# Performance work log

Hardware: AMD Instinct MI355X
Metric: run time of the kernel (lower is better)

## Reference

```python
import jax, jax.numpy as jnp
import numpy as np

SOFTCAP = 30.0

def setup_inputs() -> dict:
    key = jax.random.key(0)
    ks = jax.random.split(key, 5)
    T, D, F, E = 8192, 2048, 4096, 8
    s_in = 1.0 / np.sqrt(D)
    s_mid = 1.0 / np.sqrt(F)
    return {
        "hidden_states": jax.random.normal(ks[0], (T, D), jnp.float32),
        "gate_w": jax.random.normal(ks[1], (D, E), jnp.float32) * s_in,
        "w_gate": jax.random.normal(ks[2], (E, D, F), jnp.float32) * s_in,
        "w_up": jax.random.normal(ks[3], (E, D, F), jnp.float32) * s_in,
        "w_down": jax.random.normal(ks[4], (E, F, D), jnp.float32) * s_mid,
        "top_k": 2,
    }

def reference(hidden_states, gate_w, w_gate, w_up, w_down, top_k):
    x = hidden_states
    T = x.shape[0]
    # --- router: fp32 gate, tanh softcap, softmax ---
    logits = x.astype(jnp.float32) @ gate_w                      # [T, E]
    logits = jnp.tanh(logits / SOFTCAP) * SOFTCAP
    probs = jax.nn.softmax(logits, axis=-1)                      # [T, E]
    # --- top-k selection (weights are the softmax probs, no renorm) ---
    weights, idx = jax.lax.top_k(probs, top_k)                   # [T, k]
    combine = jnp.zeros_like(probs).at[jnp.arange(T)[:, None], idx].set(
        weights.astype(probs.dtype))                              # [T, E]
    combine = combine.astype(x.dtype)
    # --- expert MLPs: gelu(x@w_gate) * (x@w_up) @ w_down, scan over E ---
    def step(acc, ewts):
        wg, wu, wd, c = ewts                                     # [D,F],[D,F],[F,D],[T]
        h = jax.nn.gelu(x @ wg) * (x @ wu)                       # [T, F]
        return acc + c[:, None] * (h @ wd), None
    out, _ = jax.lax.scan(step, jnp.zeros_like(x),
                          (w_gate, w_up, w_down, combine.T))
    return out
```

## Files before the change

kernel.cpp:

```cpp
#include <hip/hip_runtime.h>
#include <hip/hip_bf16.h>
#include <cstdint>
#include <cstddef>

#define TNUM 8192
#define DDIM 2048
#define FDIM 4096
#define NEXP 8

typedef __attribute__((ext_vector_type(4))) float f32x4;
typedef __attribute__((ext_vector_type(4))) unsigned u32x4;
typedef __attribute__((ext_vector_type(8))) short s16x8;
typedef __attribute__((ext_vector_type(8))) __bf16 bf16x8v;

__device__ inline f32x4 mfma16(s16x8 a, s16x8 b, f32x4 c) {
  return __builtin_amdgcn_mfma_f32_16x16x32_bf16(
      __builtin_bit_cast(bf16x8v, a), __builtin_bit_cast(bf16x8v, b), c, 0, 0, 0);
}

__device__ inline unsigned short bf16r(float f) {
  union { float f; unsigned u; } x; x.f = f;
  unsigned r = x.u + 0x7fffu + ((x.u >> 16) & 1u);
  return (unsigned short)(r >> 16);
}

__device__ inline unsigned pk2(float a, float b) {
  __hip_bfloat162 h = __float22bfloat162_rn(make_float2(a, b));
  unsigned r;
  __builtin_memcpy(&r, &h, 4);
  return r;
}

__device__ inline int swz16(int row, int b) {
  return (row << 7) + (b ^ ((row & 7) << 4));
}

typedef const __attribute__((address_space(1))) void* gp_t;
typedef __attribute__((address_space(3))) void* lp_t;
__device__ inline void gl16(const void* g, void* l) {
  __builtin_amdgcn_global_load_lds((gp_t)g, (lp_t)l, 16, 0, 0);
}

#define FENCE asm volatile("" ::: "memory")

__global__ __launch_bounds__(256) void k_router(
    const float* __restrict__ x, const float* __restrict__ gw,
    int* __restrict__ top_idx, float* __restrict__ top_w, int* __restrict__ counts) {
  __shared__ float gwT[NEXP][DDIM];
  const int tid = threadIdx.x;
  for (int i = tid; i < NEXP * DDIM; i += 256) {
    int d = i >> 3, e = i & 7;
    gwT[e][d] = gw[i];
  }
  __syncthreads();
  const int lane = tid & 63;
  const int t = blockIdx.x * 4 + (tid >> 6);
  const float4* xr = (const float4*)(x + (size_t)t * DDIM);
  double acc[NEXP];
#pragma unroll
  for (int e = 0; e < NEXP; e++) acc[e] = 0.0;
  for (int d4 = lane; d4 < DDIM / 4; d4 += 64) {
    float4 xv = xr[d4];
#pragma unroll
    for (int e = 0; e < NEXP; e++) {
      float4 gv = *(const float4*)&gwT[e][d4 * 4];
      acc[e] += (double)xv.x * gv.x + (double)xv.y * gv.y +
                (double)xv.z * gv.z + (double)xv.w * gv.w;
    }
  }
#pragma unroll
  for (int e = 0; e < NEXP; e++) {
    double v = acc[e];
#pragma unroll
    for (int s = 32; s > 0; s >>= 1) v += __shfl_xor(v, s);
    acc[e] = v;
  }
  if (lane == 0) {
    int i0 = 0; double b0 = acc[0];
#pragma unroll
    for (int e = 1; e < NEXP; e++) if (acc[e] > b0) { b0 = acc[e]; i0 = e; }
    int i1 = (i0 == 0) ? 1 : 0; double b1 = acc[i1];
#pragma unroll
    for (int e = 0; e < NEXP; e++) {
      if (e == i0 || e == i1) continue;
      if (acc[e] > b1) { b1 = acc[e]; i1 = e; }
    }
    float lc[NEXP]; float mx = -1e30f;
#pragma unroll
    for (int e = 0; e < NEXP; e++) {
      lc[e] = tanhf((float)(acc[e] * (1.0 / 30.0))) * 30.0f;
      mx = lc[e] > mx ? lc[e] : mx;
    }
    float s = 0.0f;
#pragma unroll
    for (int e = 0; e < NEXP; e++) { lc[e] = expf(lc[e] - mx); s += lc[e]; }
    float inv = 1.0f / s;
    top_idx[t * 2] = i0; top_idx[t * 2 + 1] = i1;
    top_w[t * 2] = lc[i0] * inv; top_w[t * 2 + 1] = lc[i1] * inv;
    atomicAdd(&counts[i0], 1);
    atomicAdd(&counts[i1], 1);
  }
}

__global__ void k_scan(const int* __restrict__ counts, int* __restrict__ offs,
                       int* __restrict__ cursor) {
  if (threadIdx.x == 0) {
    int s = 0;
    for (int e = 0; e < NEXP; e++) { offs[e] = s; cursor[e] = s; s += counts[e]; }
    offs[NEXP] = s;
  }
}

__global__ void k_scatter(const int* __restrict__ top_idx, const float* __restrict__ top_w,
                          int* __restrict__ cursor, int* __restrict__ perm_tok,
                          float* __restrict__ perm_w) {
  int t = blockIdx.x * 256 + threadIdx.x;
#pragma unroll
  for (int k = 0; k < 2; k++) {
    int e = top_idx[t * 2 + k];
    int pos = atomicAdd(&cursor[e], 1);
    perm_tok[pos] = t;
    perm_w[pos] = top_w[t * 2 + k];
  }
}

__global__ void k_cast(const float* __restrict__ x, unsigned short* __restrict__ xb) {
  size_t i = ((size_t)blockIdx.x * 256 + threadIdx.x) * 8;
  f32x4 a = *(const f32x4*)(x + i);
  f32x4 b = *(const f32x4*)(x + i + 4);
  u32x4 v;
  v[0] = pk2(a[0], a[1]); v[1] = pk2(a[2], a[3]);
  v[2] = pk2(b[0], b[1]); v[3] = pk2(b[2], b[3]);
  *(u32x4*)(xb + i) = v;
}

__global__ __launch_bounds__(256) void k_convT(
    const float* __restrict__ src, unsigned short* __restrict__ dst,
    int K, int N, int cmap) {
  __shared__ char ct[8192];
  const int e = blockIdx.z;
  const float* src_e = src + (size_t)e * K * N;
  const int nout = cmap ? 2 * N : N;
  unsigned short* dst_e = dst + (size_t)e * nout * K;
  const int k0 = blockIdx.y * 64, n0 = blockIdx.x * 64;
  const int tid = threadIdx.x;
#pragma unroll
  for (int i = 0; i < 4; i++) {
    int idx = tid + i * 256;
    int kr = idx >> 4, f4 = idx & 15;
    f32x4 v = *(const f32x4*)(src_e + (size_t)(k0 + kr) * N + n0 + f4 * 4);
#pragma unroll
    for (int j = 0; j < 4; j++) {
      int n = f4 * 4 + j;
      *(unsigned short*)(ct + n * 128 + ((kr * 2) ^ ((n & 7) << 4))) = bf16r(v[j]);
    }
  }
  __syncthreads();
#pragma unroll
  for (int i = 0; i < 2; i++) {
    int s = tid + i * 256;
    int n = s >> 3, ks = s & 7;
    int gn = n0 + n;
    int cd = cmap ? (((gn >> 4) << 5) + (gn & 15) + (cmap == 2 ? 16 : 0)) : gn;
    s16x8 val = *(const s16x8*)(ct + n * 128 + ((ks * 16) ^ ((n & 7) << 4)));
    *(s16x8*)(dst_e + (size_t)cd * K + k0 + ks * 8) = val;
  }
}

__global__ __launch_bounds__(512, 2) void k_mlp1(
    const unsigned short* __restrict__ xb, const unsigned short* __restrict__ wguT,
    const int* __restrict__ perm_tok, const int* __restrict__ offs,
    unsigned short* __restrict__ H) {
  extern __shared__ char lds[];
  const int e = blockIdx.z;
  const int off = offs[e], cnt = offs[e + 1] - off;
  const int nb = blockIdx.x * 256;
  const unsigned short* wgu_e = wguT + (size_t)e * 2 * DDIM * FDIM;
  const int tid = threadIdx.x;
  const int lane = tid & 63;
  const int wid = tid >> 6;
  const int wr = wid >> 2, wc = wid & 3;
  const int l15 = lane & 15, lk = lane >> 4;
  const int wbase = wid * 1024;

#pragma unroll 1
  for (int mt = blockIdx.y; mt * 256 < cnt; mt += 8) {
    const unsigned short* asrc[4];
    const unsigned short* bsrc[4];
#pragma unroll
    for (int i = 0; i < 4; i++) {
      int seg = tid + i * 512;
      int m = seg >> 3, kp = (seg & 7) ^ (m & 7);
      int gm = mt * 256 + m;
      if (gm >= cnt) gm = cnt - 1;
      asrc[i] = xb + (size_t)perm_tok[off + gm] * DDIM + kp * 8;
      bsrc[i] = wgu_e + (size_t)(nb + m) * DDIM + kp * 8;
    }
    f32x4 acc[8][4];
#pragma unroll
    for (int mi = 0; mi < 8; mi++)
#pragma unroll
      for (int ni = 0; ni < 4; ni++) acc[mi][ni] = f32x4{0.f, 0.f, 0.f, 0.f};

#define STAGE1(buf, koff)                                        \
    {                                                            \
      char* As_ = lds + (buf) * 65536;                           \
      char* Bs_ = As_ + 32768;                                   \
      _Pragma("unroll") for (int i = 0; i < 4; i++) {            \
        gl16(asrc[i] + (koff), As_ + i * 8192 + wbase);          \
        gl16(bsrc[i] + (koff), Bs_ + i * 8192 + wbase);          \
      }                                                          \
    }

    STAGE1(0, 0);
    int cur = 0;
#pragma unroll 1
    for (int t = 0; t < DDIM / 64; t++) {
      if (t + 1 < DDIM / 64) {
        STAGE1(cur ^ 1, (t + 1) * 64);
        asm volatile("s_waitcnt vmcnt(8)" ::: "memory");
      } else {
        asm volatile("s_waitcnt vmcnt(0)" ::: "memory");
      }
      FENCE;
      __builtin_amdgcn_s_barrier();
      FENCE;
      {
        char* As_ = lds + cur * 65536;
        char* Bs_ = As_ + 32768;
        __builtin_amdgcn_s_setprio(1);
#pragma unroll
        for (int ks = 0; ks < 2; ks++) {
          s16x8 b[4];
#pragma unroll
          for (int ni = 0; ni < 4; ni++)
            b[ni] = *(const s16x8*)(Bs_ + swz16(wc * 64 + ni * 16 + l15, ks * 64 + lk * 16));
#pragma unroll
          for (int mih = 0; mih < 2; mih++) {
            s16x8 a[4];
#pragma unroll
            for (int mi = 0; mi < 4; mi++)
              a[mi] = *(const s16x8*)(As_ + swz16(wr * 128 + mih * 64 + mi * 16 + l15,
                                                 ks * 64 + lk * 16));
#pragma unroll
            for (int ni = 0; ni < 4; ni++)
#pragma unroll
              for (int mi = 0; mi < 4; mi++)
                acc[mih * 4 + mi][ni] = mfma16(a[mi], b[ni], acc[mih * 4 + mi][ni]);
          }
        }
        __builtin_amdgcn_s_setprio(0);
      }
      FENCE;
      __builtin_amdgcn_s_barrier();
      FENCE;
      cur ^= 1;
    }
#undef STAGE1

#pragma unroll
    for (int am = 0; am < 8; am++) {
      int rb = wr * 128 + am * 16 + lk * 4;
#pragma unroll
      for (int j = 0; j < 4; j++) {
        int gm = mt * 256 + rb + j;
        if (gm < cnt) {
          unsigned short* hrow = H + (size_t)(off + gm) * FDIM;
#pragma unroll
          for (int ni = 0; ni < 4; ni += 2) {
            int jj = (nb >> 4) + wc * 4 + ni;
            int hc = ((jj >> 1) << 4) + l15;
            float g = acc[am][ni][j];
            float u = acc[am][ni + 1][j];
            float x3 = g * g * g;
            float gl = 0.5f * g * (1.0f + tanhf(0.7978845608f * (g + 0.044715f * x3)));
            hrow[hc] = bf16r(gl * u);
          }
        }
      }
    }
  }
}

__global__ __launch_bounds__(512, 2) void k_mlp2(
    const unsigned short* __restrict__ H, const unsigned short* __restrict__ wdT,
    const int* __restrict__ perm_tok, const float* __restrict__ perm_w,
    const int* __restrict__ offs, float* __restrict__ out) {
  extern __shared__ char lds[];
  const int e = blockIdx.z;
  const int off = offs[e], cnt = offs[e + 1] - off;
  const int nb = blockIdx.x * 256;
  const unsigned short* wd_e = wdT + (size_t)e * FDIM * DDIM;
  const int tid = threadIdx.x;
  const int lane = tid & 63;
  const int wid = tid >> 6;
  const int wr = wid >> 2, wc = wid & 3;
  const int l15 = lane & 15, lk = lane >> 4;
  const int wbase = wid * 1024;

#pragma unroll 1
  for (int mt = blockIdx.y; mt * 256 < cnt; mt += 8) {
    const unsigned short* asrc[4];
    const unsigned short* bsrc[4];
#pragma unroll
    for (int i = 0; i < 4; i++) {
      int seg = tid + i * 512;
      int m = seg >> 3, kp = (seg & 7) ^ (m & 7);
      int gm = mt * 256 + m;
      if (gm >= cnt) gm = cnt - 1;
      asrc[i] = H + (size_t)(off + gm) * FDIM + kp * 8;
      bsrc[i] = wd_e + (size_t)(nb + m) * FDIM + kp * 8;
    }
    f32x4 acc[8][4];
#pragma unroll
    for (int mi = 0; mi < 8; mi++)
#pragma unroll
      for (int ni = 0; ni < 4; ni++) acc[mi][ni] = f32x4{0.f, 0.f, 0.f, 0.f};

#define STAGE2(buf, koff)                                        \
    {                                                            \
      char* As_ = lds + (buf) * 65536;                           \
      char* Bs_ = As_ + 32768;                                   \
      _Pragma("unroll") for (int i = 0; i < 4; i++) {            \
        gl16(asrc[i] + (koff), As_ + i * 8192 + wbase);          \
        gl16(bsrc[i] + (koff), Bs_ + i * 8192 + wbase);          \
      }                                                          \
    }

    STAGE2(0, 0);
    int cur = 0;
#pragma unroll 1
    for (int t = 0; t < FDIM / 64; t++) {
      if (t + 1 < FDIM / 64) {
        STAGE2(cur ^ 1, (t + 1) * 64);
        asm volatile("s_waitcnt vmcnt(8)" ::: "memory");
      } else {
        asm volatile("s_waitcnt vmcnt(0)" ::: "memory");
      }
      FENCE;
      __builtin_amdgcn_s_barrier();
      FENCE;
      {
        char* As_ = lds + cur * 65536;
        char* Bs_ = As_ + 32768;
        __builtin_amdgcn_s_setprio(1);
#pragma unroll
        for (int ks = 0; ks < 2; ks++) {
          s16x8 b[4];
#pragma unroll
          for (int ni = 0; ni < 4; ni++)
            b[ni] = *(const s16x8*)(Bs_ + swz16(wc * 64 + ni * 16 + l15, ks * 64 + lk * 16));
#pragma unroll
          for (int mih = 0; mih < 2; mih++) {
            s16x8 a[4];
#pragma unroll
            for (int mi = 0; mi < 4; mi++)
              a[mi] = *(const s16x8*)(As_ + swz16(wr * 128 + mih * 64 + mi * 16 + l15,
                                                 ks * 64 + lk * 16));
#pragma unroll
            for (int ni = 0; ni < 4; ni++)
#pragma unroll
              for (int mi = 0; mi < 4; mi++)
                acc[mih * 4 + mi][ni] = mfma16(a[mi], b[ni], acc[mih * 4 + mi][ni]);
          }
        }
        __builtin_amdgcn_s_setprio(0);
      }
      FENCE;
      __builtin_amdgcn_s_barrier();
      FENCE;
      cur ^= 1;
    }
#undef STAGE2

#pragma unroll
    for (int am = 0; am < 8; am++) {
      int rb = wr * 128 + am * 16 + lk * 4;
#pragma unroll
      for (int j = 0; j < 4; j++) {
        int gm = mt * 256 + rb + j;
        if (gm < cnt) {
          int tok = perm_tok[off + gm];
          float w = perm_w[off + gm];
          float* orow = out + (size_t)tok * DDIM + nb + wc * 64 + l15;
#pragma unroll
          for (int ni = 0; ni < 4; ni++) atomicAdd(&orow[ni * 16], w * acc[am][ni][j]);
        }
      }
    }
  }
}

extern "C" void kernel_launch(void* const* d_in, const int* in_sizes, int n_in,
                              void* d_out, int out_size, void* d_ws, size_t ws_size,
                              hipStream_t stream) {
  const float* x = (const float*)d_in[0];
  const float* gw = (const float*)d_in[1];
  const float* wgate = (const float*)d_in[2];
  const float* wup = (const float*)d_in[3];
  const float* wdown = (const float*)d_in[4];
  float* out = (float*)d_out;

  const size_t XB_B = 33554432;
  const size_t H_B = 134217728;
  const size_t WGU_B = 268435456;
  const size_t WD_B = 134217728;

  char* ws = (char*)d_ws;
  unsigned short* xb = (unsigned short*)ws;
  unsigned short* H = (unsigned short*)(ws + XB_B);
  unsigned short* wguT = (unsigned short*)(ws + XB_B + H_B);
  unsigned short* wdT = (unsigned short*)(ws + XB_B + H_B + WGU_B);
  char* meta = ws + XB_B + H_B + WGU_B + WD_B;
  int* counts = (int*)(meta);
  int* offs = (int*)(meta + 64);
  int* cursor = (int*)(meta + 128);
  int* top_idx = (int*)(meta + 256);
  float* top_w = (float*)(meta + 256 + 65536);
  int* perm_tok = (int*)(meta + 256 + 131072);
  float* perm_w = (float*)(meta + 256 + 196608);

  (void)hipFuncSetAttribute((const void*)k_mlp1,
                            hipFuncAttributeMaxDynamicSharedMemorySize, 131072);
  (void)hipFuncSetAttribute((const void*)k_mlp2,
                            hipFuncAttributeMaxDynamicSharedMemorySize, 131072);

  (void)hipMemsetAsync(counts, 0, 64, stream);
  (void)hipMemsetAsync(d_out, 0, (size_t)TNUM * DDIM * 4, stream);
  k_router<<<TNUM / 4, 256, 0, stream>>>(x, gw, top_idx, top_w, counts);
  k_scan<<<1, 64, 0, stream>>>(counts, offs, cursor);
  k_scatter<<<TNUM / 256, 256, 0, stream>>>(top_idx, top_w, cursor, perm_tok, perm_w);
  k_cast<<<(TNUM * DDIM / 8) / 256, 256, 0, stream>>>(x, xb);
  k_convT<<<dim3(FDIM / 64, DDIM / 64, NEXP), 256, 0, stream>>>(wgate, wguT, DDIM, FDIM, 1);
  k_convT<<<dim3(FDIM / 64, DDIM / 64, NEXP), 256, 0, stream>>>(wup, wguT, DDIM, FDIM, 2);
  k_convT<<<dim3(DDIM / 64, FDIM / 64, NEXP), 256, 0, stream>>>(wdown, wdT, FDIM, DDIM, 0);
  k_mlp1<<<dim3(2 * FDIM / 256, 8, NEXP), 512, 131072, stream>>>(xb, wguT, perm_tok, offs, H);
  k_mlp2<<<dim3(DDIM / 256, 8, NEXP), 512, 131072, stream>>>(H, wdT, perm_tok, perm_w, offs, out);
}
```

Before: 1.593 ms.

## Restructure GEMM main loop into quadrant phases with one barrier per tile

Both expert GEMM kernels now use a new K-loop schedule. The next tile's global-to-LDS loads are issued first, and the 256x256 tile is then computed as four 128x128 quadrant phases that load A and B fragments just in time. A single vmcnt(0) wait and one barrier per iteration replace the previous wait-then-barrier-compute-barrier pattern, which removes one barrier per K step. LDS staging is reorganised so each wave loads contiguous rows per quadrant, and fragment lifetimes are shorter, which lowers register pressure. The risk is that waiting for all loads at the end of every iteration exposes memory latency if the compute phases are too short to hide it.

```diff
diff --git a/kernel.cpp b/kernel.cpp
--- a/kernel.cpp
+++ b/kernel.cpp
@@ -166,6 +166,37 @@
     *(s16x8*)(dst_e + (size_t)cd * K + k0 + ks * 8) = val;
   }
 }
+
+#define PHASE(MIH, NIH, BUF)                                                   \
+  {                                                                            \
+    char* Ab_ = lds + (BUF) * 65536;                                           \
+    char* Bb_ = Ab_ + 32768;                                                   \
+    __builtin_amdgcn_s_setprio(1);                                             \
+    _Pragma("unroll") for (int kk = 0; kk < 2; kk++) {                         \
+      s16x8 b0_ = *(const s16x8*)(Bb_ +                                        \
+          swz16(wc * 64 + (NIH) * 32 + l15, kk * 64 + lk * 16));               \
+      s16x8 b1_ = *(const s16x8*)(Bb_ +                                        \
+          swz16(wc * 64 + (NIH) * 32 + 16 + l15, kk * 64 + lk * 16));          \
+      _Pragma("unroll") for (int mi = 0; mi < 4; mi++) {                       \
+        s16x8 a_ = *(const s16x8*)(Ab_ +                                       \
+            swz16(wr * 128 + (MIH) * 64 + mi * 16 + l15, kk * 64 + lk * 16));  \
+        acc[(MIH) * 4 + mi][(NIH) * 2 + 0] =                                   \
+            mfma16(a_, b0_, acc[(MIH) * 4 + mi][(NIH) * 2 + 0]);               \
+        acc[(MIH) * 4 + mi][(NIH) * 2 + 1] =                                   \
+            mfma16(a_, b1_, acc[(MIH) * 4 + mi][(NIH) * 2 + 1]);               \
+      }                                                                        \
+    }                                                                          \
+    __builtin_amdgcn_s_setprio(0);                                             \
+  }
+
+#define STAGEU(U, TN)                                                          \
+  {                                                                            \
+    char* db_ = lds + ((TN) & 1) * 65536 + (U) * 16384 + wid * 2048;           \
+    gl16(sp[U][0] + (size_t)(TN) * 64, db_);                                   \
+    gl16(sp[U][1] + (size_t)(TN) * 64, db_ + 1024);                            \
+  }
+
+#define VMC(N) asm volatile("s_waitcnt vmcnt(" #N ")" ::: "memory")
 
 __global__ __launch_bounds__(512, 2) void k_mlp1(
     const unsigned short* __restrict__ xb, const unsigned short* __restrict__ wguT,
@@ -181,20 +212,22 @@
   const int wid = tid >> 6;
   const int wr = wid >> 2, wc = wid & 3;
   const int l15 = lane & 15, lk = lane >> 4;
-  const int wbase = wid * 1024;
+  const int NT = DDIM / 64;
 
 #pragma unroll 1
   for (int mt = blockIdx.y; mt * 256 < cnt; mt += 8) {
-    const unsigned short* asrc[4];
-    const unsigned short* bsrc[4];
-#pragma unroll
-    for (int i = 0; i < 4; i++) {
-      int seg = tid + i * 512;
-      int m = seg >> 3, kp = (seg & 7) ^ (m & 7);
-      int gm = mt * 256 + m;
-      if (gm >= cnt) gm = cnt - 1;
-      asrc[i] = xb + (size_t)perm_tok[off + gm] * DDIM + kp * 8;
-      bsrc[i] = wgu_e + (size_t)(nb + m) * DDIM + kp * 8;
+    const unsigned short* sp[4][2];
+#pragma unroll
+    for (int c = 0; c < 2; c++) {
+      int r = wid * 16 + c * 8 + (lane >> 3);
+      int k16 = (lane & 7) ^ (r & 7);
+      int glo = mt * 256 + r, ghi = mt * 256 + 128 + r;
+      if (glo >= cnt) glo = cnt - 1;
+      if (ghi >= cnt) ghi = cnt - 1;
+      sp[0][c] = xb + (size_t)perm_tok[off + glo] * DDIM + k16 * 8;
+      sp[1][c] = xb + (size_t)perm_tok[off + ghi] * DDIM + k16 * 8;
+      sp[2][c] = wgu_e + (size_t)(nb + r) * DDIM + k16 * 8;
+      sp[3][c] = wgu_e + (size_t)(nb + 128 + r) * DDIM + k16 * 8;
     }
     f32x4 acc[8][4];
 #pragma unroll
@@ -202,61 +235,26 @@
 #pragma unroll
       for (int ni = 0; ni < 4; ni++) acc[mi][ni] = f32x4{0.f, 0.f, 0.f, 0.f};
 
-#define STAGE1(buf, koff)                                        \
-    {                                                            \
-      char* As_ = lds + (buf) * 65536;                           \
-      char* Bs_ = As_ + 32768;                                   \
-      _Pragma("unroll") for (int i = 0; i < 4; i++) {            \
-        gl16(asrc[i] + (koff), As_ + i * 8192 + wbase);          \
-        gl16(bsrc[i] + (koff), Bs_ + i * 8192 + wbase);          \
-      }                                                          \
-    }
-
-    STAGE1(0, 0);
-    int cur = 0;
+    STAGEU(0, 0) STAGEU(1, 0) STAGEU(2, 0) STAGEU(3, 0)
+    VMC(0);
+    FENCE;
+    __builtin_amdgcn_s_barrier();
+    FENCE;
 #pragma unroll 1
-    for (int t = 0; t < DDIM / 64; t++) {
-      if (t + 1 < DDIM / 64) {
-        STAGE1(cur ^ 1, (t + 1) * 64);
-        asm volatile("s_waitcnt vmcnt(8)" ::: "memory");
-      } else {
-        asm volatile("s_waitcnt vmcnt(0)" ::: "memory");
+    for (int t = 0; t < NT; t++) {
+      const int buf = t & 1;
+      if (t + 1 < NT) {
+        STAGEU(0, t + 1) STAGEU(1, t + 1) STAGEU(2, t + 1) STAGEU(3, t + 1)
       }
+      PHASE(0, 0, buf);
+      PHASE(0, 1, buf);
+      PHASE(1, 0, buf);
+      PHASE(1, 1, buf);
+      VMC(0);
       FENCE;
       __builtin_amdgcn_s_barrier();
       FENCE;
-      {
-        char* As_ = lds + cur * 65536;
-        char* Bs_ = As_ + 32768;
-        __builtin_amdgcn_s_setprio(1);
-#pragma unroll
-        for (int ks = 0; ks < 2; ks++) {
-          s16x8 b[4];
-#pragma unroll
-          for (int ni = 0; ni < 4; ni++)
-            b[ni] = *(const s16x8*)(Bs_ + swz16(wc * 64 + ni * 16 + l15, ks * 64 + lk * 16));
-#pragma unroll
-          for (int mih = 0; mih < 2; mih++) {
-            s16x8 a[4];
-#pragma unroll
-            for (int mi = 0; mi < 4; mi++)
-              a[mi] = *(const s16x8*)(As_ + swz16(wr * 128 + mih * 64 + mi * 16 + l15,
-                                                 ks * 64 + lk * 16));
-#pragma unroll
-            for (int ni = 0; ni < 4; ni++)
-#pragma unroll
-              for (int mi = 0; mi < 4; mi++)
-                acc[mih * 4 + mi][ni] = mfma16(a[mi], b[ni], acc[mih * 4 + mi][ni]);
-          }
-        }
-        __builtin_amdgcn_s_setprio(0);
-      }
-      FENCE;
-      __builtin_amdgcn_s_barrier();
-      FENCE;
-      cur ^= 1;
-    }
-#undef STAGE1
+    }
 
 #pragma unroll
     for (int am = 0; am < 8; am++) {
@@ -296,20 +294,22 @@
   const int wid = tid >> 6;
   const int wr = wid >> 2, wc = wid & 3;
   const int l15 = lane & 15, lk = lane >> 4;
-  const int wbase = wid * 1024;
+  const int NT = FDIM / 64;
 
 #pragma unroll 1
   for (int mt = blockIdx.y; mt * 256 < cnt; mt += 8) {
-    const unsigned short* asrc[4];
-    const unsigned short* bsrc[4];
-#pragma unroll
-    for (int i = 0; i < 4; i++) {
-      int seg = tid + i * 512;
-      int m = seg >> 3, kp = (seg & 7) ^ (m & 7);
-      int gm = mt * 256 + m;
-      if (gm >= cnt) gm = cnt - 1;
-      asrc[i] = H + (size_t)(off + gm) * FDIM + kp * 8;
-      bsrc[i] = wd_e + (size_t)(nb + m) * FDIM + kp * 8;
+    const unsigned short* sp[4][2];
+#pragma unroll
+    for (int c = 0; c < 2; c++) {
+      int r = wid * 16 + c * 8 + (lane >> 3);
+      int k16 = (lane & 7) ^ (r & 7);
+      int glo = mt * 256 + r, ghi = mt * 256 + 128 + r;
+      if (glo >= cnt) glo = cnt - 1;
+      if (ghi >= cnt) ghi = cnt - 1;
+      sp[0][c] = H + (size_t)(off + glo) * FDIM + k16 * 8;
+      sp[1][c] = H + (size_t)(off + ghi) * FDIM + k16 * 8;
+      sp[2][c] = wd_e + (size_t)(nb + r) * FDIM + k16 * 8;
+      sp[3][c] = wd_e + (size_t)(nb + 128 + r) * FDIM + k16 * 8;
     }
     f32x4 acc[8][4];
 #pragma unroll
@@ -317,61 +317,26 @@
 #pragma unroll
       for (int ni = 0; ni < 4; ni++) acc[mi][ni] = f32x4{0.f, 0.f, 0.f, 0.f};
 
-#define STAGE2(buf, koff)                                        \
-    {                                                            \
-      char* As_ = lds + (buf) * 65536;                           \
-      char* Bs_ = As_ + 32768;                                   \
-      _Pragma("unroll") for (int i = 0; i < 4; i++) {            \
-        gl16(asrc[i] + (koff), As_ + i * 8192 + wbase);          \
-        gl16(bsrc[i] + (koff), Bs_ + i * 8192 + wbase);          \
-      }                                                          \
-    }
-
-    STAGE2(0, 0);
-    int cur = 0;
+    STAGEU(0, 0) STAGEU(1, 0) STAGEU(2, 0) STAGEU(3, 0)
+    VMC(0);
+    FENCE;
+    __builtin_amdgcn_s_barrier();
+    FENCE;
 #pragma unroll 1
-    for (int t = 0; t < FDIM / 64; t++) {
-      if (t + 1 < FDIM / 64) {
-        STAGE2(cur ^ 1, (t + 1) * 64);
-        asm volatile("s_waitcnt vmcnt(8)" ::: "memory");
-      } else {
-        asm volatile("s_waitcnt vmcnt(0)" ::: "memory");
+    for (int t = 0; t < NT; t++) {
+      const int buf = t & 1;
+      if (t + 1 < NT) {
+        STAGEU(0, t + 1) STAGEU(1, t + 1) STAGEU(2, t + 1) STAGEU(3, t + 1)
       }
+      PHASE(0, 0, buf);
+      PHASE(0, 1, buf);
+      PHASE(1, 0, buf);
+      PHASE(1, 1, buf);
+      VMC(0);
       FENCE;
       __builtin_amdgcn_s_barrier();
       FENCE;
-      {
-        char* As_ = lds + cur * 65536;
-        char* Bs_ = As_ + 32768;
-        __builtin_amdgcn_s_setprio(1);
-#pragma unroll
-        for (int ks = 0; ks < 2; ks++) {
-          s16x8 b[4];
-#pragma unroll
-          for (int ni = 0; ni < 4; ni++)
-            b[ni] = *(const s16x8*)(Bs_ + swz16(wc * 64 + ni * 16 + l15, ks * 64 + lk * 16));
-#pragma unroll
-          for (int mih = 0; mih < 2; mih++) {
-            s16x8 a[4];
-#pragma unroll
-            for (int mi = 0; mi < 4; mi++)
-              a[mi] = *(const s16x8*)(As_ + swz16(wr * 128 + mih * 64 + mi * 16 + l15,
-                                                 ks * 64 + lk * 16));
-#pragma unroll
-            for (int ni = 0; ni < 4; ni++)
-#pragma unroll
-              for (int mi = 0; mi < 4; mi++)
-                acc[mih * 4 + mi][ni] = mfma16(a[mi], b[ni], acc[mih * 4 + mi][ni]);
-          }
-        }
-        __builtin_amdgcn_s_setprio(0);
-      }
-      FENCE;
-      __builtin_amdgcn_s_barrier();
-      FENCE;
-      cur ^= 1;
-    }
-#undef STAGE2
+    }
 
 #pragma unroll
     for (int am = 0; am < 8; am++) {
```

Measured after the change: 1.555 ms. -2.3%, faster.
